# Kernel tuning notes

Measured on AMD Instinct MI355X. Metric: run time of the kernel, lower is better.

The kernel has to match this reference:

```python
import jax, jax.numpy as jnp
import numpy as np

B, T, D, H, O = 256, 512, 256, 512, 1


def setup_inputs() -> dict:
    key = jax.random.key(0)
    ks = jax.random.split(key, 4)
    x = jax.random.normal(ks[0], (B, T, D), dtype=jnp.float32)
    W = jax.random.normal(ks[1], (D, 3 * H), dtype=jnp.float32) * (1.0 / np.sqrt(D))
    U = jax.random.normal(ks[2], (H, 3 * H), dtype=jnp.float32) * (1.0 / np.sqrt(H))
    b = jnp.zeros((3 * H,), dtype=jnp.float32)
    Wd = jax.random.normal(ks[3], (H, O), dtype=jnp.float32) * (1.0 / np.sqrt(H))
    bd = jnp.zeros((O,), dtype=jnp.float32)
    return {"x": x, "W": W, "U": U, "b": b, "Wd": Wd, "bd": bd}


def _gru_last_hidden(x, W, U, b):
    # x: [B, T, D]; returns final hidden state [B, H]
    units = U.shape[0]
    bz, br, bn = b[:units], b[units:2 * units], b[2 * units:]
    Uzr, Un = U[:, :2 * units], U[:, 2 * units:]
    # precompute input projections for all timesteps: [B, T, 3H] -> [T, B, 3H]
    gx = jnp.einsum('btd,dk->tbk', x, W)

    def step(h, gx_t):
        gxz = gx_t[:, :units]
        gxr = gx_t[:, units:2 * units]
        gxn = gx_t[:, 2 * units:]
        gh_zr = h @ Uzr                      # [B, 2H]
        z = jax.nn.sigmoid(gxz + gh_zr[:, :units] + bz)
        r = jax.nn.sigmoid(gxr + gh_zr[:, units:] + br)
        n = jnp.tanh(gxn + (r * h) @ Un + bn)
        h_new = z * h + (1.0 - z) * n
        return h_new, None

    h0 = jnp.zeros((x.shape[0], units), dtype=x.dtype)
    h_last, _ = jax.lax.scan(step, h0, gx)
    return h_last


def reference(x, W, U, b, Wd, bd):
    h_last = _gru_last_hidden(x, W, U, b)  # [B, H]
    return h_last @ Wd + bd                # [B, O]
```

## Files before the change

kernel.cpp:

```cpp
#include <hip/hip_runtime.h>
#include <hip/hip_bf16.h>

typedef __attribute__((ext_vector_type(8))) short short8;
typedef __attribute__((ext_vector_type(4))) float f32x4;
typedef __attribute__((ext_vector_type(4))) unsigned int u32x4;
typedef __attribute__((ext_vector_type(4))) unsigned short u16x4;

#define T_STEPS 512
#define DIM_D 256
#define DIM_H 512
#define NGROUP 8
#define NCOL 32
#define BB 32
#define SLC 16
#define FSTRIDE 32

__device__ __forceinline__ unsigned short f2bf(float f) {
  union { float f; unsigned u; } v; v.f = f;
  unsigned r = v.u + 0x7fffu + ((v.u >> 16) & 1u);
  return (unsigned short)(r >> 16);
}
__device__ __forceinline__ float sigm(float x) { return 1.0f / (1.0f + __expf(-x)); }
__device__ __forceinline__ float tanh_fast(float x) { return 2.0f / (1.0f + __expf(-2.0f * x)) - 1.0f; }

__device__ __forceinline__ void ldg8_bypass(const void* p, u32x4* o) {
  asm volatile(
      "global_load_dwordx4 %0, %8, off sc0 sc1\n\t"
      "global_load_dwordx4 %1, %8, off offset:16 sc0 sc1\n\t"
      "global_load_dwordx4 %2, %8, off offset:32 sc0 sc1\n\t"
      "global_load_dwordx4 %3, %8, off offset:48 sc0 sc1\n\t"
      "global_load_dwordx4 %4, %8, off offset:64 sc0 sc1\n\t"
      "global_load_dwordx4 %5, %8, off offset:80 sc0 sc1\n\t"
      "global_load_dwordx4 %6, %8, off offset:96 sc0 sc1\n\t"
      "global_load_dwordx4 %7, %8, off offset:112 sc0 sc1\n\t"
      "s_waitcnt vmcnt(0)"
      : "=&v"(o[0]), "=&v"(o[1]), "=&v"(o[2]), "=&v"(o[3]),
        "=&v"(o[4]), "=&v"(o[5]), "=&v"(o[6]), "=&v"(o[7])
      : "v"(p)
      : "memory");
}
__device__ __forceinline__ void stg_u16_bypass(void* p, unsigned v) {
  asm volatile("global_store_short %0, %1, off sc0 sc1" :: "v"(p), "v"(v) : "memory");
}
__device__ __forceinline__ void stg_u32_bypass(void* p, unsigned v) {
  asm volatile("global_store_dword %0, %1, off sc0 sc1" :: "v"(p), "v"(v) : "memory");
}
__device__ __forceinline__ unsigned ldg_u32_bypass(const void* p) {
  unsigned v;
  asm volatile("global_load_dword %0, %1, off sc0 sc1\n\ts_waitcnt vmcnt(0)"
               : "=v"(v) : "v"(p) : "memory");
  return v;
}

__global__ void k_init(unsigned* hx_u32, unsigned* flags) {
  int i = blockIdx.x * 256 + threadIdx.x;
  if (i < 65536) hx_u32[i] = 0u;
  if (i < 2 * NGROUP * 64 * FSTRIDE) flags[i] = 0u;
}

__global__ void k_packW(const float* __restrict__ W, unsigned short* __restrict__ Wt) {
  int n = blockIdx.x, k = threadIdx.x;
  Wt[n * 256 + k] = f2bf(W[(size_t)k * 1536 + n]);
}

__global__ void k_packU(const float* __restrict__ U, unsigned short* __restrict__ Ut) {
  int n = blockIdx.x;
  for (int k = threadIdx.x; k < 512; k += 256)
    Ut[n * 512 + k] = f2bf(U[(size_t)k * 1536 + n]);
}

__global__ void k_out(const float* __restrict__ part, const float* __restrict__ bd,
                      float* __restrict__ out) {
  int b = threadIdx.x;
  float s = bd[0];
  for (int c = 0; c < 32; c++) s += part[c * 256 + b];
  out[b] = s;
}

__global__ void __launch_bounds__(256, 1)
k_gru(const float* __restrict__ x, const float* __restrict__ bias,
      const float* __restrict__ Wd,
      const unsigned short* __restrict__ Wt, const unsigned short* __restrict__ Ut,
      unsigned short* hx, unsigned short* rhx,
      float* part, unsigned* flags) {
  extern __shared__ char smem[];
  char* sUzr = smem;
  char* sUn  = smem + 32768;
  char* sW   = smem + 49152;
  char* sH   = smem + 73728;
  char* sX   = smem + 106496;
  float* sHM = (float*)(smem + 122880);

  const int tid = threadIdx.x;
  const int bid = blockIdx.x;
  const int g = bid & 7;
  const int c = bid >> 3;
  const int w = tid >> 6;
  const int l = tid & 63;
  const int lrow = l & 15;
  const int lk = l >> 4;
  const int n0 = c * SLC;
  const int mt = w & 1;
  const bool zw = (w < 2);

  unsigned* fA = flags + g * 64 * FSTRIDE;
  unsigned* fB = flags + NGROUP * 64 * FSTRIDE + g * 64 * FSTRIDE;

  unsigned short* hx_g  = hx  + (size_t)g * (BB * DIM_H);
  unsigned short* rhx_g = rhx + (size_t)g * (BB * DIM_H);

  for (int q = tid; q < 2048; q += 256) {
    int n = q >> 6, ch = q & 63;
    int grow = (n < 16) ? (n0 + n) : (DIM_H + n0 + (n - 16));
    u32x4 v = *(const u32x4*)(Ut + (size_t)grow * DIM_H + ch * 8);
    *(u32x4*)(sUzr + n * 1024 + ((ch * 16) ^ ((n & 7) << 4))) = v;
  }
  for (int q = tid; q < 1024; q += 256) {
    int n = q >> 6, ch = q & 63;
    int grow = 2 * DIM_H + n0 + n;
    u32x4 v = *(const u32x4*)(Ut + (size_t)grow * DIM_H + ch * 8);
    *(u32x4*)(sUn + n * 1024 + ((ch * 16) ^ ((n & 7) << 4))) = v;
  }
  for (int q = tid; q < 1536; q += 256) {
    int n = q >> 5, ch = q & 31;
    int grow = (n < 16) ? (n0 + n) : (n < 32 ? (DIM_H + n0 + (n - 16))
                                             : (2 * DIM_H + n0 + (n - 32)));
    u32x4 v = *(const u32x4*)(Wt + (size_t)grow * DIM_D + ch * 8);
    *(u32x4*)(sW + n * 512 + ((ch * 16) ^ ((n & 7) << 4))) = v;
  }
  sHM[tid] = 0.0f; sHM[tid + 256] = 0.0f;
  const float bz_l = bias[n0 + lrow];
  const float br_l = bias[DIM_H + n0 + lrow];
  const float bn_l = bias[2 * DIM_H + n0 + lrow];
  __syncthreads();

  f32x4 azr, an;

  auto stage_x = [&](int t) {
    const int xr = tid >> 3;
    const int xj = (tid & 7) * 32;
    const float* xp = x + ((size_t)(g * BB + xr) * T_STEPS + t) * DIM_D + xj;
#pragma unroll
    for (int i = 0; i < 8; i++) {
      float4 v = ((const float4*)xp)[i];
      u16x4 h4 = { f2bf(v.x), f2bf(v.y), f2bf(v.z), f2bf(v.w) };
      int kb = (xj + i * 4) * 2;
      *(u16x4*)(sX + xr * 512 + (kb ^ ((xr & 7) << 4))) = h4;
    }
  };

  auto w_mfma = [&]() {
    float bini = zw ? bz_l : br_l;
    f32x4 t0 = { bini, bini, bini, bini };
    azr = t0;
    f32x4 t1 = { bn_l, bn_l, bn_l, bn_l };
    an = t1;
    const int arow = mt * 16 + lrow;
    const int nzr = zw ? lrow : (16 + lrow);
    const int nnn = 32 + lrow;
#pragma unroll
    for (int ks = 0; ks < 8; ks++) {
      int kb = ks * 64 + lk * 16;
      short8 a = *(const short8*)(sX + arow * 512 + (kb ^ ((arow & 7) << 4)));
      short8 b0 = *(const short8*)(sW + nzr * 512 + (kb ^ ((nzr & 7) << 4)));
      azr = __builtin_amdgcn_mfma_f32_16x16x32_bf16(a, b0, azr, 0, 0, 0);
      if (zw) {
        short8 b1 = *(const short8*)(sW + nnn * 512 + (kb ^ ((nnn & 7) << 4)));
        an = __builtin_amdgcn_mfma_f32_16x16x32_bf16(a, b1, an, 0, 0, 0);
      }
    }
  };

  auto stage_gl = [&](const unsigned short* src_base) {
    const int hr = tid >> 3;
    const int hc = (tid & 7) * 128;
    const char* s0 = (const char*)(src_base + hr * DIM_H) + hc;
    u32x4 v[8];
    ldg8_bypass(s0, v);
    char* dst = sH + hr * 1024;
    const int sw = (hr & 7) << 4;
#pragma unroll
    for (int i = 0; i < 8; i++)
      *(u32x4*)(dst + ((hc + i * 16) ^ sw)) = v[i];
  };

  auto uzr_mfma = [&]() {
    const int arow = mt * 16 + lrow;
    const int n = zw ? lrow : (16 + lrow);
#pragma unroll
    for (int ks = 0; ks < 16; ks++) {
      int kb = ks * 64 + lk * 16;
      short8 a = *(const short8*)(sH + arow * 1024 + (kb ^ ((arow & 7) << 4)));
      short8 b8 = *(const short8*)(sUzr + n * 1024 + (kb ^ ((n & 7) << 4)));
      azr = __builtin_amdgcn_mfma_f32_16x16x32_bf16(a, b8, azr, 0, 0, 0);
    }
  };

  auto un_mfma = [&]() {
    const int arow = mt * 16 + lrow;
#pragma unroll
    for (int ks = 0; ks < 16; ks++) {
      int kb = ks * 64 + lk * 16;
      short8 a = *(const short8*)(sH + arow * 1024 + (kb ^ ((arow & 7) << 4)));
      short8 b8 = *(const short8*)(sUn + lrow * 1024 + (kb ^ ((lrow & 7) << 4)));
      an = __builtin_amdgcn_mfma_f32_16x16x32_bf16(a, b8, an, 0, 0, 0);
    }
  };

  stage_x(0);
  __syncthreads();
  w_mfma();

  for (int t = 0; t < T_STEPS; t++) {
    const unsigned e = (unsigned)(t + 1);

    stage_gl(hx_g);
    __syncthreads();
    uzr_mfma();
    if (!zw) {
#pragma unroll
      for (int j = 0; j < 4; j++) {
        int row = mt * 16 + lk * 4 + j;
        float rv = sigm(azr[j]);
        stg_u16_bypass(rhx_g + row * DIM_H + n0 + lrow,
                       (unsigned)f2bf(rv * sHM[row * 16 + lrow]));
      }
      asm volatile("s_waitcnt vmcnt(0)" ::: "memory");
      if (l == 0) stg_u32_bypass(fA + ((c << 1) | (w & 1)) * FSTRIDE, e);
    } else if (w == 0) {
      while (ldg_u32_bypass(fA + l * FSTRIDE) < e) __builtin_amdgcn_s_sleep(1);
    }
    __syncthreads();

    stage_gl(rhx_g);
    __syncthreads();
    if (zw) {
      un_mfma();
#pragma unroll
      for (int j = 0; j < 4; j++) {
        int row = mt * 16 + lk * 4 + j;
        float zv = sigm(azr[j]);
        float nv = tanh_fast(an[j]);
        float hv = sHM[row * 16 + lrow];
        float hn = zv * hv + (1.0f - zv) * nv;
        sHM[row * 16 + lrow] = hn;
        if (t + 1 < T_STEPS)
          stg_u16_bypass(hx_g + row * DIM_H + n0 + lrow, (unsigned)f2bf(hn));
      }
      if (t + 1 < T_STEPS) {
        asm volatile("s_waitcnt vmcnt(0)" ::: "memory");
        if (l == 0) stg_u32_bypass(fB + ((c << 1) | w) * FSTRIDE, e);
      }
    }
    if (t + 1 == T_STEPS) { __syncthreads(); break; }
    stage_x(t + 1);
    __syncthreads();
    w_mfma();
    if (w == 2) {
      while (ldg_u32_bypass(fB + l * FSTRIDE) < e) __builtin_amdgcn_s_sleep(1);
    }
    __syncthreads();
  }

  if (tid < BB) {
    float s = 0.0f;
#pragma unroll
    for (int i = 0; i < SLC; i++) s += sHM[tid * 16 + i] * Wd[n0 + i];
    part[c * 256 + g * BB + tid] = s;
  }
}

extern "C" void kernel_launch(void* const* d_in, const int* in_sizes, int n_in,
                              void* d_out, int out_size, void* d_ws, size_t ws_size,
                              hipStream_t stream) {
  const float* x    = (const float*)d_in[0];
  const float* W    = (const float*)d_in[1];
  const float* U    = (const float*)d_in[2];
  const float* bias = (const float*)d_in[3];
  const float* Wd   = (const float*)d_in[4];
  const float* bd   = (const float*)d_in[5];
  float* out = (float*)d_out;
  char* ws = (char*)d_ws;

  unsigned short* Wt  = (unsigned short*)(ws + 0);
  unsigned short* Ut  = (unsigned short*)(ws + 786432);
  unsigned short* hx  = (unsigned short*)(ws + 2359296);
  unsigned short* rhx = (unsigned short*)(ws + 2621440);
  float* part         = (float*)(ws + 2883584);
  unsigned* flags     = (unsigned*)(ws + 2916352);

  hipFuncSetAttribute((const void*)k_gru, hipFuncAttributeMaxDynamicSharedMemorySize, 124928);

  k_init<<<256, 256, 0, stream>>>((unsigned*)hx, flags);
  k_packW<<<1536, 256, 0, stream>>>(W, Wt);
  k_packU<<<1536, 256, 0, stream>>>(U, Ut);
  k_gru<<<256, 256, 124928, stream>>>(x, bias, Wd, Wt, Ut, hx, rhx, part, flags);
  k_out<<<1, 256, 0, stream>>>(part, bd, out);
}
```

Baseline: 5.234 ms.

## Replace centralized flag spin with per-thread distributed polling and packed atomic stores

Each thread now polls only the producer flags covering the slice of h it will load, immediately before its load, instead of one wave spinning on all flags followed by a block barrier. Hidden-state and r*h stores are packed into 32-bit atomic swaps via a lane shuffle, halving the number of global store instructions. The x-projection staging is also overlapped with the flag publish, which removes one barrier per step. The trade-off is more polling traffic per block and a bounded poll count (MAXP) that silently proceeds if the limit is reached.

```diff
diff --git a/kernel.cpp b/kernel.cpp
--- a/kernel.cpp
+++ b/kernel.cpp
@@ -14,6 +14,7 @@
 #define BB 32
 #define SLC 16
 #define FSTRIDE 32
+#define MAXP 16384
 
 __device__ __forceinline__ unsigned short f2bf(float f) {
   union { float f; unsigned u; } v; v.f = f;
@@ -39,17 +40,8 @@
       : "v"(p)
       : "memory");
 }
-__device__ __forceinline__ void stg_u16_bypass(void* p, unsigned v) {
-  asm volatile("global_store_short %0, %1, off sc0 sc1" :: "v"(p), "v"(v) : "memory");
-}
-__device__ __forceinline__ void stg_u32_bypass(void* p, unsigned v) {
-  asm volatile("global_store_dword %0, %1, off sc0 sc1" :: "v"(p), "v"(v) : "memory");
-}
-__device__ __forceinline__ unsigned ldg_u32_bypass(const void* p) {
-  unsigned v;
-  asm volatile("global_load_dword %0, %1, off sc0 sc1\n\ts_waitcnt vmcnt(0)"
-               : "=v"(v) : "v"(p) : "memory");
-  return v;
+__device__ __forceinline__ void atom_st_u32(unsigned* p, unsigned v) {
+  asm volatile("global_atomic_swap %0, %1, off" :: "v"(p), "v"(v) : "memory");
 }
 
 __global__ void k_init(unsigned* hx_u32, unsigned* flags) {
@@ -108,6 +100,8 @@
 
   unsigned short* hx_g  = hx  + (size_t)g * (BB * DIM_H);
   unsigned short* rhx_g = rhx + (size_t)g * (BB * DIM_H);
+  unsigned* hx32_g  = (unsigned*)hx_g;
+  unsigned* rhx32_g = (unsigned*)rhx_g;
 
   for (int q = tid; q < 2048; q += 256) {
     int n = q >> 6, ch = q & 63;
@@ -171,17 +165,33 @@
     }
   };
 
-  auto stage_gl = [&](const unsigned short* src_base) {
+  auto pollload = [&](const unsigned short* src_base, unsigned* f, unsigned e) {
     const int hr = tid >> 3;
-    const int hc = (tid & 7) * 128;
-    const char* s0 = (const char*)(src_base + hr * DIM_H) + hc;
+    const int ck = tid & 7;
+    const int half = hr >> 4;
+    const unsigned* fp = f + (((unsigned)(ck << 3)) | half) * FSTRIDE;
+    for (int it = 0; it < MAXP; ++it) {
+      unsigned a0, a1, a2, a3;
+      asm volatile(
+          "global_load_dword %0, %4, off sc0 sc1\n\t"
+          "global_load_dword %1, %4, off offset:256 sc0 sc1\n\t"
+          "global_load_dword %2, %4, off offset:512 sc0 sc1\n\t"
+          "global_load_dword %3, %4, off offset:768 sc0 sc1\n\t"
+          "s_waitcnt vmcnt(0)"
+          : "=&v"(a0), "=&v"(a1), "=&v"(a2), "=&v"(a3)
+          : "v"(fp)
+          : "memory");
+      if (a0 >= e && a1 >= e && a2 >= e && a3 >= e) break;
+      __builtin_amdgcn_s_sleep(1);
+    }
+    const char* s0 = (const char*)(src_base + hr * DIM_H) + ck * 128;
     u32x4 v[8];
     ldg8_bypass(s0, v);
     char* dst = sH + hr * 1024;
     const int sw = (hr & 7) << 4;
 #pragma unroll
     for (int i = 0; i < 8; i++)
-      *(u32x4*)(dst + ((hc + i * 16) ^ sw)) = v[i];
+      *(u32x4*)(dst + ((ck * 128 + i * 16) ^ sw)) = v[i];
   };
 
   auto uzr_mfma = [&]() {
@@ -212,9 +222,9 @@
   w_mfma();
 
   for (int t = 0; t < T_STEPS; t++) {
-    const unsigned e = (unsigned)(t + 1);
-
-    stage_gl(hx_g);
+    const unsigned e1 = (unsigned)(t + 1);
+
+    pollload(hx_g, fB, (unsigned)t);
     __syncthreads();
     uzr_mfma();
     if (!zw) {
@@ -222,17 +232,19 @@
       for (int j = 0; j < 4; j++) {
         int row = mt * 16 + lk * 4 + j;
         float rv = sigm(azr[j]);
-        stg_u16_bypass(rhx_g + row * DIM_H + n0 + lrow,
-                       (unsigned)f2bf(rv * sHM[row * 16 + lrow]));
+        unsigned mv = (unsigned)f2bf(rv * sHM[row * 16 + lrow]);
+        unsigned nb = (unsigned)__shfl_xor((int)mv, 1, 64) & 0xFFFFu;
+        if (!(lrow & 1))
+          atom_st_u32(rhx32_g + row * 256 + ((n0 + lrow) >> 1), mv | (nb << 16));
       }
+    }
+    __syncthreads();
+    if (!zw) {
       asm volatile("s_waitcnt vmcnt(0)" ::: "memory");
-      if (l == 0) stg_u32_bypass(fA + ((c << 1) | (w & 1)) * FSTRIDE, e);
-    } else if (w == 0) {
-      while (ldg_u32_bypass(fA + l * FSTRIDE) < e) __builtin_amdgcn_s_sleep(1);
-    }
-    __syncthreads();
-
-    stage_gl(rhx_g);
+      if (l == 0) atom_st_u32(fA + ((c << 1) | mt) * FSTRIDE, e1);
+    }
+
+    pollload(rhx_g, fA, e1);
     __syncthreads();
     if (zw) {
       un_mfma();
@@ -244,22 +256,21 @@
         float hv = sHM[row * 16 + lrow];
         float hn = zv * hv + (1.0f - zv) * nv;
         sHM[row * 16 + lrow] = hn;
-        if (t + 1 < T_STEPS)
-          stg_u16_bypass(hx_g + row * DIM_H + n0 + lrow, (unsigned)f2bf(hn));
+        if (t + 1 < T_STEPS) {
+          unsigned mv = (unsigned)f2bf(hn);
+          unsigned nb = (unsigned)__shfl_xor((int)mv, 1, 64) & 0xFFFFu;
+          if (!(lrow & 1))
+            atom_st_u32(hx32_g + row * 256 + ((n0 + lrow) >> 1), mv | (nb << 16));
+        }
       }
-      if (t + 1 < T_STEPS) {
-        asm volatile("s_waitcnt vmcnt(0)" ::: "memory");
-        if (l == 0) stg_u32_bypass(fB + ((c << 1) | w) * FSTRIDE, e);
-      }
-    }
-    if (t + 1 == T_STEPS) { __syncthreads(); break; }
-    stage_x(t + 1);
+    }
+    if (t + 1 < T_STEPS) stage_x(t + 1);
+    if (zw && t + 1 < T_STEPS) {
+      asm volatile("s_waitcnt vmcnt(0)" ::: "memory");
+      if (l == 0) atom_st_u32(fB + ((c << 1) | mt) * FSTRIDE, e1);
+    }
     __syncthreads();
-    w_mfma();
-    if (w == 2) {
-      while (ldg_u32_bypass(fB + l * FSTRIDE) < e) __builtin_amdgcn_s_sleep(1);
-    }
-    __syncthreads();
+    if (t + 1 < T_STEPS) w_mfma();
   }
 
   if (tid < BB) {
```

Result: faster. 4.958 ms (median of 2 runs) (-5.3%).
